# Performance work log

Hardware: AMD Instinct MI355X
Metric: run time of the kernel (lower is better)

The kernel has to match this reference:

```python
import jax, jax.numpy as jnp
import numpy as np
from jax import lax

TAU = 2.0
V_TH = 1.0
SG_ALPHA = 4.0  # spikingjelly default sigmoid surrogate alpha


def lif_multistep(x):
    """Multi-step LIF with hard reset to 0, v_init=0, detach_reset=True.
    x: (T, ...). Returns binary spikes (same shape), with sigmoid surrogate
    gradient injected via straight-through estimator.
    """
    def step(v, xt):
        h = v + (xt - v) / TAU                      # membrane charge
        s_hard = (h >= V_TH).astype(h.dtype)        # heaviside spike
        sur = jax.nn.sigmoid(SG_ALPHA * (h - V_TH))  # surrogate for grad
        s = s_hard + (sur - lax.stop_gradient(sur))  # fwd=hard, bwd=surrogate
        v_next = h * (1.0 - lax.stop_gradient(s))    # hard reset, detached
        return v_next, s
    _, spikes = lax.scan(step, jnp.zeros_like(x[0]), x)
    return spikes


def setup_inputs() -> dict:
    key = jax.random.key(0)
    ks = jax.random.split(key, 6)
    T, B, N, D = 4, 16, 197, 512
    w_std = 1.0 / np.sqrt(D)
    return {
        "x":  jax.random.normal(ks[0], (T, B, N, D), dtype=jnp.float32),
        "Wq": jax.random.normal(ks[1], (D, D), dtype=jnp.float32) * w_std,
        "Wk": jax.random.normal(ks[2], (D, D), dtype=jnp.float32) * w_std,
        "Wv": jax.random.normal(ks[3], (D, D), dtype=jnp.float32) * w_std,
        "Wp": jax.random.normal(ks[4], (D, D), dtype=jnp.float32) * w_std,
        "bp": jnp.zeros((D,), dtype=jnp.float32),
    }


def reference(x, Wq, Wk, Wv, Wp, bp):
    T, B, N, D = x.shape
    H = 8
    dh = D // H
    scale = dh ** -0.5

    # QKV projections (nn.Linear: x @ W.T, no bias)
    q = jnp.einsum('tbnd,ed->tbne', x, Wq)
    k = jnp.einsum('tbnd,ed->tbne', x, Wk)
    v = jnp.einsum('tbnd,ed->tbne', x, Wv)

    # LIF spiking over timestep dim T -> binary spike tensors
    qs = lif_multistep(q).reshape(T, B, N, H, dh).transpose(0, 1, 3, 2, 4)
    ks_ = lif_multistep(k).reshape(T, B, N, H, dh).transpose(0, 1, 3, 2, 4)
    vs = lif_multistep(v).reshape(T, B, N, H, dh).transpose(0, 1, 3, 2, 4)

    # spike-driven attention: binary matmul, no softmax
    attn = jnp.einsum('tbhnd,tbhmd->tbhnm', qs, ks_) * scale  # (T,B,H,N,N)
    attn_map = lax.stop_gradient(attn)
    out = jnp.einsum('tbhnm,tbhmd->tbhnd', attn, vs)          # (T,B,H,N,dh)
    out = out.transpose(0, 1, 3, 2, 4).reshape(T, B, N, D)

    # output projection + LIF
    out = jnp.einsum('tbnd,ed->tbne', out, Wp) + bp
    out = lif_multistep(out)
    return out, attn_map
```

## Files before the change

kernel.cpp:

```cpp
#include <hip/hip_runtime.h>
#include <stdint.h>

#define T_ 4
#define B_ 16
#define N_ 197
#define D_ 512
#define H_ 8
#define DH 64
#define BN_ (B_*N_)
#define PLANE (BN_*D_)
#define M_ (T_*BN_)
#define TENSOR_ELEMS (T_*PLANE)
#define WELEMS (D_*D_)
#define MH (M_*H_)
#define FLAG_TOL 6e-3f
#define NFW3 (3*PLANE/64)
#define NFWP (PLANE/64)

typedef __attribute__((ext_vector_type(8))) short short8v;
typedef __attribute__((ext_vector_type(8))) _Float16 f16x8;
typedef __attribute__((ext_vector_type(4))) float f32x4;
typedef __attribute__((ext_vector_type(16))) float f32x16;
typedef __attribute__((ext_vector_type(4))) unsigned short ushort4v;
typedef unsigned long long u64;
typedef unsigned int u32;

__device__ __forceinline__ ushort f16_bits(float f) {
    _Float16 h = (_Float16)f;
    return __builtin_bit_cast(unsigned short, h);
}
__device__ __forceinline__ float f16_val(ushort u) {
    return (float)__builtin_bit_cast(_Float16, u);
}

__device__ __forceinline__ void gload16(const void* g, void* l) {
    __builtin_amdgcn_global_load_lds(
        (const __attribute__((address_space(1))) unsigned int*)g,
        (__attribute__((address_space(3))) unsigned int*)l, 16, 0, 0);
}

__device__ __forceinline__ short8v unpack8(u32 bits) {
    short8v r;
    #pragma unroll
    for (int j = 0; j < 8; ++j)
        r[j] = (short)(((bits >> j) & 1u) ? 0x3F80 : 0);
    return r;
}

__global__ void cvt16(const float* __restrict__ src, ushort* __restrict__ dst, int n)
{
    int i = (blockIdx.x*256 + threadIdx.x)*4;
    if (i >= n) return;
    float4 v = *(const float4*)(src + i);
    ushort4v o;
    o[0] = f16_bits(v.x); o[1] = f16_bits(v.y);
    o[2] = f16_bits(v.z); o[3] = f16_bits(v.w);
    *(ushort4v*)(dst + i) = o;
}

__global__ __launch_bounds__(256)
void gemm_qkv_lif(const ushort* __restrict__ xh, const ushort* __restrict__ w3h,
                  u64* __restrict__ bits3, u64* __restrict__ fmap3)
{
    __shared__ __align__(16) ushort smem[32768];
    const int tid = threadIdx.x;
    const int lane = tid & 63, wn = tid >> 6;
    const int l31 = lane & 31, lg = lane >> 5;
    const int nyz = 12, nz = 3;

    int nwg = gridDim.x, orig = blockIdx.x;
    int q8 = nwg >> 3, r8 = nwg & 7, xcd = orig & 7, loc = orig >> 3;
    int wg = (xcd < r8 ? xcd*(q8+1) : r8*(q8+1) + (xcd-r8)*q8) + loc;
    int bx = wg / nyz, yz = wg - bx*nyz;
    int by = yz / nz,  z  = yz - by*nz;

    const int bm0 = bx * 32;
    const int bn0 = by * 128;
    const ushort* Wz = w3h + (size_t)z * WELEMS;

    f32x16 acc[4];
    #pragma unroll
    for (int t = 0; t < 4; ++t)
        #pragma unroll
        for (int r = 0; r < 16; ++r) acc[t][r] = 0.f;

    auto STAGE = [&](int buf, int kt) {
        #pragma unroll
        for (int i = 0; i < 8; ++i) {
            const int q = ((i & 3) << 8) | tid;
            const int row = q & 127, c = q >> 7;
            ushort* dst = smem + buf*16384 + ((i >> 2) << 13) + q*8;
            if (i < 4) {
                int t = row >> 5, r32 = row & 31;
                if (bm0 + r32 < BN_)
                    gload16(xh + ((size_t)(t*BN_ + bm0 + r32)*D_ + kt + c*8), dst);
            } else {
                gload16(Wz + ((size_t)(bn0 + row)*D_ + kt + c*8), dst);
            }
        }
    };
    auto COMPUTE = [&](int buf) {
        const ushort* base = smem + buf*16384;
        #pragma unroll
        for (int s = 0; s < 4; ++s) {
            const int cA = (s << 1) | lg;
            f16x8 bv = *(const f16x8*)&base[8192 + (cA*128 + wn*32 + l31)*8];
            #pragma unroll
            for (int t = 0; t < 4; ++t) {
                f16x8 av = *(const f16x8*)&base[(cA*128 + t*32 + l31)*8];
                acc[t] = __builtin_amdgcn_mfma_f32_32x32x16_f16(av, bv, acc[t], 0, 0, 0);
            }
        }
    };

    STAGE(0, 0);
    __syncthreads();
    int cur = 0;
    #pragma unroll
    for (int k64 = 0; k64 < 8; ++k64) {
        if (k64 < 7) STAGE(cur ^ 1, (k64 + 1)*64);
        COMPUTE(cur);
        __syncthreads();
        cur ^= 1;
    }

    u32* sp = (u32*)smem;
    u32* fl = (u32*)smem + 512;
    #pragma unroll
    for (int r = 0; r < 16; ++r) {
        bool s[4]; bool fg = false; float v = 0.f;
        #pragma unroll
        for (int t = 0; t < 4; ++t) {
            float h = v + (acc[t][r] - v)*0.5f;
            s[t] = h >= 1.0f;
            fg |= fabsf(h - 1.0f) < FLAG_TOL;
            v = s[t] ? 0.f : h;
        }
        #pragma unroll
        for (int t = 0; t < 4; ++t) {
            u64 m = __ballot(s[t]);
            if (lane == 0) {
                sp[((wn*4 + t)*16 + r)*2 + 0] = (u32)m;
                sp[((wn*4 + t)*16 + r)*2 + 1] = (u32)(m >> 32);
            }
        }
        u64 fm = __ballot(fg);
        if (lane == 0) {
            fl[(wn*16 + r)*2 + 0] = (u32)fm;
            fl[(wn*16 + r)*2 + 1] = (u32)(fm >> 32);
        }
    }
    __syncthreads();
    {
        int t = tid >> 6, row32 = (tid >> 1) & 31, hl = tid & 1;
        int rr = (row32 & 3) | ((row32 >> 3) << 2);
        int lgg = (row32 >> 2) & 1;
        u64 word = (u64)sp[(((2*hl)*4 + t)*16 + rr)*2 + lgg]
                 | ((u64)sp[(((2*hl+1)*4 + t)*16 + rr)*2 + lgg] << 32);
        if (bm0 + row32 < BN_)
            bits3[(size_t)z*MH + (size_t)(t*BN_ + bm0 + row32)*H_ + (bn0 >> 6) + hl] = word;
        if (tid < 64) {
            int rowf = tid >> 1, hlf = tid & 1;
            int rf = (rowf & 3) | ((rowf >> 3) << 2);
            int lgf = (rowf >> 2) & 1;
            u64 fw = (u64)fl[((2*hlf)*16 + rf)*2 + lgf]
                   | ((u64)fl[((2*hlf+1)*16 + rf)*2 + lgf] << 32);
            if (bm0 + rowf < BN_)
                fmap3[(size_t)z*NFWP + (size_t)(bm0 + rowf)*8 + (bn0 >> 6) + hlf] = fw;
        }
    }
}

__global__ __launch_bounds__(256)
void gemm_proj_lif(const ushort* __restrict__ oh, const ushort* __restrict__ wph,
                   const float* __restrict__ bias, float* __restrict__ outp,
                   u64* __restrict__ fmapp)
{
    __shared__ __align__(16) ushort smem[32768];
    const int tid = threadIdx.x;
    const int lane = tid & 63, wn = tid >> 6;
    const int l31 = lane & 31, lg = lane >> 5;
    const int nyz = 4;

    int nwg = gridDim.x, orig = blockIdx.x;
    int q8 = nwg >> 3, r8 = nwg & 7, xcd = orig & 7, loc = orig >> 3;
    int wg = (xcd < r8 ? xcd*(q8+1) : r8*(q8+1) + (xcd-r8)*q8) + loc;
    int bx = wg / nyz, by = wg - bx*nyz;

    const int bm0 = bx * 32, bn0 = by * 128;

    f32x16 acc[4];
    #pragma unroll
    for (int t = 0; t < 4; ++t)
        #pragma unroll
        for (int r = 0; r < 16; ++r) acc[t][r] = 0.f;

    auto STAGE = [&](int buf, int kt) {
        #pragma unroll
        for (int i = 0; i < 8; ++i) {
            const int q = ((i & 3) << 8) | tid;
            const int row = q & 127, c = q >> 7;
            ushort* dst = smem + buf*16384 + ((i >> 2) << 13) + q*8;
            if (i < 4) {
                int t = row >> 5, r32 = row & 31;
                if (bm0 + r32 < BN_)
                    gload16(oh + ((size_t)(t*BN_ + bm0 + r32)*D_ + kt + c*8), dst);
            } else {
                gload16(wph + ((size_t)(bn0 + row)*D_ + kt + c*8), dst);
            }
        }
    };
    auto COMPUTE = [&](int buf) {
        const ushort* base = smem + buf*16384;
        #pragma unroll
        for (int s = 0; s < 4; ++s) {
            const int cA = (s << 1) | lg;
            f16x8 bv = *(const f16x8*)&base[8192 + (cA*128 + wn*32 + l31)*8];
            #pragma unroll
            for (int t = 0; t < 4; ++t) {
                f16x8 av = *(const f16x8*)&base[(cA*128 + t*32 + l31)*8];
                acc[t] = __builtin_amdgcn_mfma_f32_32x32x16_f16(av, bv, acc[t], 0, 0, 0);
            }
        }
    };

    STAGE(0, 0);
    __syncthreads();
    int cur = 0;
    #pragma unroll
    for (int k64 = 0; k64 < 8; ++k64) {
        if (k64 < 7) STAGE(cur ^ 1, (k64 + 1)*64);
        COMPUTE(cur);
        __syncthreads();
        cur ^= 1;
    }

    const int gcol = bn0 + wn*32 + l31;
    const float bb = bias[gcol];
    u32* fl = (u32*)smem;
    #pragma unroll
    for (int r = 0; r < 16; ++r) {
        const int row32 = (r & 3) + 8*(r >> 2) + 4*lg;
        const bool live = bm0 + row32 < BN_;
        bool fg = false; float v = 0.f;
        #pragma unroll
        for (int t = 0; t < 4; ++t) {
            float h = v + ((acc[t][r] + bb) - v)*0.5f;
            bool st = h >= 1.0f;
            fg |= fabsf(h - 1.0f) < FLAG_TOL;
            if (live)
                outp[(size_t)t*PLANE + (size_t)(bm0 + row32)*D_ + gcol] = st ? 1.0f : 0.0f;
            v = st ? 0.f : h;
        }
        u64 fm = __ballot(fg);
        if (lane == 0) {
            fl[(wn*16 + r)*2 + 0] = (u32)fm;
            fl[(wn*16 + r)*2 + 1] = (u32)(fm >> 32);
        }
    }
    __syncthreads();
    if (tid < 64) {
        int rowf = tid >> 1, hlf = tid & 1;
        int rf = (rowf & 3) | ((rowf >> 3) << 2);
        int lgf = (rowf >> 2) & 1;
        u64 fw = (u64)fl[((2*hlf)*16 + rf)*2 + lgf]
               | ((u64)fl[((2*hlf+1)*16 + rf)*2 + lgf] << 32);
        if (bm0 + rowf < BN_)
            fmapp[(size_t)(bm0 + rowf)*8 + (bn0 >> 6) + hlf] = fw;
    }
}

__global__ __launch_bounds__(256)
void fixup_qkv(const float* __restrict__ x,
               const float* __restrict__ Wq, const float* __restrict__ Wk,
               const float* __restrict__ Wv,
               u64* __restrict__ bits3, const u64* __restrict__ flagmap)
{
    const int lane = threadIdx.x & 63;
    const int wv = blockIdx.x*4 + (threadIdx.x >> 6);
    const int nw = gridDim.x*4;
    for (int w = wv; w < NFW3; w += nw) {
        u64 fm = flagmap[w];
        while (fm) {
            int bit = __ffsll((long long)fm) - 1;
            fm &= fm - 1;
            int id = (w << 6) + bit;
            int tsr = id / PLANE;
            int rem = id - tsr*PLANE;
            int r = rem >> 9, e = rem & (D_-1);
            const float* W = (tsr==0) ? Wq : (tsr==1 ? Wk : Wv);
            const float* wr = W + (size_t)e*D_;
            u64* bits = bits3 + (size_t)tsr*MH;
            float wv8[8];
            #pragma unroll
            for (int i = 0; i < 8; ++i) wv8[i] = wr[lane + 64*i];
            double dots[T_];
            #pragma unroll
            for (int t = 0; t < T_; ++t) {
                const float* xr = x + (size_t)(t*BN_ + r)*D_;
                float xv8[8];
                #pragma unroll
                for (int i = 0; i < 8; ++i) xv8[i] = xr[lane + 64*i];
                double p = 0.0;
                #pragma unroll
                for (int i = 0; i < 8; ++i) p += (double)xv8[i]*(double)wv8[i];
                dots[t] = p;
            }
            #pragma unroll
            for (int off = 32; off > 0; off >>= 1)
                #pragma unroll
                for (int t = 0; t < T_; ++t)
                    dots[t] += __shfl_down(dots[t], off);
            if (lane == 0) {
                double v = 0.0;
                u64 b = 1ull << (e & 63);
                #pragma unroll
                for (int t = 0; t < T_; ++t) {
                    double hh = v + (dots[t] - v)/2.0;
                    bool s = hh >= 1.0;
                    size_t wd = (size_t)(t*BN_ + r)*H_ + (e >> 6);
                    if (s) atomicOr(&bits[wd], b);
                    else   atomicAnd(&bits[wd], ~b);
                    v = s ? 0.0 : hh;
                }
            }
        }
    }
}

#define JP 224
#define VSTR 232

__global__ __launch_bounds__(256)
void attn_fused(const u64* __restrict__ qbits, const u64* __restrict__ kbits,
                const u64* __restrict__ vbits,
                float* __restrict__ attn_out, ushort* __restrict__ of16)
{
    __shared__ ushort Vt[DH][VSTR];
    __shared__ ushort Ss[4][16][VSTR];
    int tb = blockIdx.x, h = blockIdx.y;
    int tid = threadIdx.x, wave = tid >> 6, lane = tid & 63;

    for (int idx = tid; idx < JP*16; idx += 256) {
        int j = idx >> 4, d4 = (idx & 15) << 2;
        ushort vv[4] = {0,0,0,0};
        if (j < N_) {
            u64 vw = vbits[((size_t)tb*N_ + j)*H_ + h];
            #pragma unroll
            for (int r = 0; r < 4; ++r)
                vv[r] = ((vw >> (d4+r)) & 1ull) ? 0x3F80 : 0;
        }
        Vt[d4+0][j]=vv[0]; Vt[d4+1][j]=vv[1]; Vt[d4+2][j]=vv[2]; Vt[d4+3][j]=vv[3];
    }
    for (int idx = lane; idx < 16*16; idx += 64)
        Ss[wave][idx >> 4][208 + (idx & 15)] = 0;
    __syncthreads();

    const int il = lane & 15, kk = (lane >> 4) << 3, ig = (lane >> 4) << 2;
    const size_t amap = ((size_t)tb*H_ + h)*(size_t)(N_*N_);

    for (int it = wave; it < 13; it += 4) {
        int i0 = it << 4;
        int qrow = i0 + il;
        u64 qw = (qrow < N_) ? qbits[((size_t)tb*N_ + qrow)*H_ + h] : 0ull;
        short8v a0 = unpack8((u32)(qw >> kk));
        short8v a1 = unpack8((u32)((qw >> 32) >> kk));
        for (int jt = 0; jt < 13; ++jt) {
            int j0 = jt << 4, jrow = j0 + il;
            u64 kw = (jrow < N_) ? kbits[((size_t)tb*N_ + jrow)*H_ + h] : 0ull;
            short8v b0 = unpack8((u32)(kw >> kk));
            short8v b1 = unpack8((u32)((kw >> 32) >> kk));
            f32x4 c = {0.f, 0.f, 0.f, 0.f};
            c = __builtin_amdgcn_mfma_f32_16x16x32_bf16(a0, b0, c, 0, 0, 0);
            c = __builtin_amdgcn_mfma_f32_16x16x32_bf16(a1, b1, c, 0, 0, 0);
            int j = j0 + il;
            #pragma unroll
            for (int r = 0; r < 4; ++r) {
                float sv = c[r]*0.125f;
                int i = i0 + ig + r;
                if (i < N_ && j < N_)
                    attn_out[amap + (size_t)i*N_ + j] = sv;
                Ss[wave][ig + r][j] = (ushort)(__float_as_uint(sv) >> 16);
            }
        }
        f32x4 o[4];
        #pragma unroll
        for (int dt = 0; dt < 4; ++dt) o[dt] = (f32x4){0.f,0.f,0.f,0.f};
        #pragma unroll
        for (int kt = 0; kt < 7; ++kt) {
            short8v a = *(const short8v*)&Ss[wave][il][kt*32 + kk];
            #pragma unroll
            for (int dt = 0; dt < 4; ++dt) {
                short8v b = *(const short8v*)&Vt[dt*16 + il][kt*32 + kk];
                o[dt] = __builtin_amdgcn_mfma_f32_16x16x32_bf16(a, b, o[dt], 0, 0, 0);
            }
        }
        #pragma unroll
        for (int dt = 0; dt < 4; ++dt)
            #pragma unroll
            for (int r = 0; r < 4; ++r) {
                int i = i0 + ig + r;
                if (i < N_)
                    of16[((size_t)tb*N_ + i)*D_ + (size_t)h*DH + dt*16 + il] =
                        f16_bits(o[dt][r]);
            }
    }
}

__global__ __launch_bounds__(256)
void fixup_proj(const ushort* __restrict__ of16, const float* __restrict__ Wp,
                const float* __restrict__ bp, float* __restrict__ outp,
                const u64* __restrict__ flagmap)
{
    const int lane = threadIdx.x & 63;
    const int wv = blockIdx.x*4 + (threadIdx.x >> 6);
    const int nw = gridDim.x*4;
    for (int w = wv; w < NFWP; w += nw) {
        u64 fm = flagmap[w];
        while (fm) {
            int bit = __ffsll((long long)fm) - 1;
            fm &= fm - 1;
            int rem = (w << 6) + bit;
            int r = rem >> 9, e = rem & (D_-1);
            const float* wr = Wp + (size_t)e*D_;
            float wv8[8];
            #pragma unroll
            for (int i = 0; i < 8; ++i) wv8[i] = wr[lane + 64*i];
            double dots[T_];
            #pragma unroll
            for (int t = 0; t < T_; ++t) {
                const ushort* ar = of16 + (size_t)(t*BN_ + r)*D_;
                float av8[8];
                #pragma unroll
                for (int i = 0; i < 8; ++i) av8[i] = f16_val(ar[lane + 64*i]);
                double p = 0.0;
                #pragma unroll
                for (int i = 0; i < 8; ++i) p += (double)av8[i]*(double)wv8[i];
                dots[t] = p;
            }
            #pragma unroll
            for (int off = 32; off > 0; off >>= 1)
                #pragma unroll
                for (int t = 0; t < T_; ++t)
                    dots[t] += __shfl_down(dots[t], off);
            if (lane == 0) {
                double v = 0.0;
                #pragma unroll
                for (int t = 0; t < T_; ++t) {
                    double xt = dots[t] + (double)bp[e];
                    double h = v + (xt - v)/2.0;
                    bool s = h >= 1.0;
                    outp[(size_t)t*PLANE + rem] = s ? 1.0f : 0.0f;
                    v = s ? 0.0 : h;
                }
            }
        }
    }
}

extern "C" void kernel_launch(void* const* d_in, const int* in_sizes, int n_in,
                              void* d_out, int out_size, void* d_ws, size_t ws_size,
                              hipStream_t stream)
{
    const float* x  = (const float*)d_in[0];
    const float* Wq = (const float*)d_in[1];
    const float* Wk = (const float*)d_in[2];
    const float* Wv = (const float*)d_in[3];
    const float* Wp = (const float*)d_in[4];
    const float* bp = (const float*)d_in[5];
    float* out_spk  = (float*)d_out;
    float* attn_out = (float*)d_out + TENSOR_ELEMS;

    char* ws = (char*)d_ws;
    const size_t BUFB = (size_t)TENSOR_ELEMS * sizeof(float);
    if (ws_size < 4*BUFB) return;
    ushort* of16 = (ushort*)(ws + 2*BUFB);
    char* r3 = ws + 3*BUFB;
    ushort* xh   = (ushort*)r3;
    ushort* w3h  = (ushort*)(r3 + (13u<<20));
    ushort* wph  = (ushort*)(r3 + (15u<<20));
    u64*    bits3 = (u64*)(r3 + (16u<<20));
    u64*    qbits = bits3;
    u64*    kbits = bits3 + MH;
    u64*    vbits = bits3 + 2*(size_t)MH;
    u64*    fmap3 = (u64*)(r3 + (19u<<20));
    u64*    fmapp = (u64*)(r3 + (20u<<20));

    cvt16<<<TENSOR_ELEMS/1024, 256, 0, stream>>>(x, xh, TENSOR_ELEMS);
    cvt16<<<WELEMS/1024, 256, 0, stream>>>(Wq, w3h,            WELEMS);
    cvt16<<<WELEMS/1024, 256, 0, stream>>>(Wk, w3h +   WELEMS, WELEMS);
    cvt16<<<WELEMS/1024, 256, 0, stream>>>(Wv, w3h + 2*WELEMS, WELEMS);
    cvt16<<<WELEMS/1024, 256, 0, stream>>>(Wp, wph,            WELEMS);

    gemm_qkv_lif<<<99*12, 256, 0, stream>>>(xh, w3h, bits3, fmap3);
    fixup_qkv<<<2048, 256, 0, stream>>>(x, Wq, Wk, Wv, bits3, fmap3);

    attn_fused<<<dim3(T_*B_, H_), 256, 0, stream>>>(
        qbits, kbits, vbits, attn_out, of16);

    gemm_proj_lif<<<99*4, 256, 0, stream>>>(of16, wph, bp, out_spk, fmapp);
    fixup_proj<<<1024, 256, 0, stream>>>(of16, Wp, bp, out_spk, fmapp);
}
```

Baseline: 168.9 us.

## Halve GEMM K-tile for occupancy, merge convert launches, coalesce attention map stores

Both fused GEMM+LIF kernels now stage 32-wide K slices instead of 64-wide ones, halving shared memory, and request 4 blocks per CU through launch bounds. The loop runs twice as many stages, each with more barriers per unit of work. The five fp16 conversion launches are merged into one kernel that picks its source buffer by block index, which removes launch overhead. The attention map is now written from the LDS score tile in row-contiguous, lane-coalesced stores instead of scattered per-fragment stores. This relies on the bf16-truncated scores being exact, which holds because they are binary dot products times 0.125.

Result: faster. 159.7 us (-5.4%).

```diff
diff --git a/kernel.cpp b/kernel.cpp
--- a/kernel.cpp
+++ b/kernel.cpp
@@ -47,10 +47,23 @@
     return r;
 }
 
-__global__ void cvt16(const float* __restrict__ src, ushort* __restrict__ dst, int n)
-{
-    int i = (blockIdx.x*256 + threadIdx.x)*4;
-    if (i >= n) return;
+#define NBX (TENSOR_ELEMS/1024)
+#define NBW (WELEMS/1024)
+
+__global__ void cvt_all(const float* __restrict__ x,  const float* __restrict__ Wq,
+                        const float* __restrict__ Wk, const float* __restrict__ Wv,
+                        const float* __restrict__ Wp,
+                        ushort* __restrict__ xh, ushort* __restrict__ w3h,
+                        ushort* __restrict__ wph)
+{
+    int b = blockIdx.x;
+    const float* src; ushort* dst; int base;
+    if      (b < NBX)         { src = x;  dst = xh;             base = b; }
+    else if (b < NBX + NBW)   { src = Wq; dst = w3h;            base = b - NBX; }
+    else if (b < NBX + 2*NBW) { src = Wk; dst = w3h + WELEMS;   base = b - NBX - NBW; }
+    else if (b < NBX + 3*NBW) { src = Wv; dst = w3h + 2*WELEMS; base = b - NBX - 2*NBW; }
+    else                      { src = Wp; dst = wph;            base = b - NBX - 3*NBW; }
+    int i = (base*256 + threadIdx.x)*4;
     float4 v = *(const float4*)(src + i);
     ushort4v o;
     o[0] = f16_bits(v.x); o[1] = f16_bits(v.y);
@@ -58,11 +71,11 @@
     *(ushort4v*)(dst + i) = o;
 }
 
-__global__ __launch_bounds__(256)
+__global__ __launch_bounds__(256, 4)
 void gemm_qkv_lif(const ushort* __restrict__ xh, const ushort* __restrict__ w3h,
                   u64* __restrict__ bits3, u64* __restrict__ fmap3)
 {
-    __shared__ __align__(16) ushort smem[32768];
+    __shared__ __align__(16) ushort smem[16384];
     const int tid = threadIdx.x;
     const int lane = tid & 63, wn = tid >> 6;
     const int l31 = lane & 31, lg = lane >> 5;
@@ -86,11 +99,11 @@
 
     auto STAGE = [&](int buf, int kt) {
         #pragma unroll
-        for (int i = 0; i < 8; ++i) {
-            const int q = ((i & 3) << 8) | tid;
+        for (int i = 0; i < 4; ++i) {
+            const int q = ((i & 1) << 8) | tid;
             const int row = q & 127, c = q >> 7;
-            ushort* dst = smem + buf*16384 + ((i >> 2) << 13) + q*8;
-            if (i < 4) {
+            ushort* dst = smem + buf*8192 + ((i >> 1) << 12) + q*8;
+            if (i < 2) {
                 int t = row >> 5, r32 = row & 31;
                 if (bm0 + r32 < BN_)
                     gload16(xh + ((size_t)(t*BN_ + bm0 + r32)*D_ + kt + c*8), dst);
@@ -100,11 +113,11 @@
         }
     };
     auto COMPUTE = [&](int buf) {
-        const ushort* base = smem + buf*16384;
-        #pragma unroll
-        for (int s = 0; s < 4; ++s) {
+        const ushort* base = smem + buf*8192;
+        #pragma unroll
+        for (int s = 0; s < 2; ++s) {
             const int cA = (s << 1) | lg;
-            f16x8 bv = *(const f16x8*)&base[8192 + (cA*128 + wn*32 + l31)*8];
+            f16x8 bv = *(const f16x8*)&base[4096 + (cA*128 + wn*32 + l31)*8];
             #pragma unroll
             for (int t = 0; t < 4; ++t) {
                 f16x8 av = *(const f16x8*)&base[(cA*128 + t*32 + l31)*8];
@@ -117,8 +130,8 @@
     __syncthreads();
     int cur = 0;
     #pragma unroll
-    for (int k64 = 0; k64 < 8; ++k64) {
-        if (k64 < 7) STAGE(cur ^ 1, (k64 + 1)*64);
+    for (int k32 = 0; k32 < 16; ++k32) {
+        if (k32 < 15) STAGE(cur ^ 1, (k32 + 1)*32);
         COMPUTE(cur);
         __syncthreads();
         cur ^= 1;
@@ -171,12 +184,12 @@
     }
 }
 
-__global__ __launch_bounds__(256)
+__global__ __launch_bounds__(256, 4)
 void gemm_proj_lif(const ushort* __restrict__ oh, const ushort* __restrict__ wph,
                    const float* __restrict__ bias, float* __restrict__ outp,
                    u64* __restrict__ fmapp)
 {
-    __shared__ __align__(16) ushort smem[32768];
+    __shared__ __align__(16) ushort smem[16384];
     const int tid = threadIdx.x;
     const int lane = tid & 63, wn = tid >> 6;
     const int l31 = lane & 31, lg = lane >> 5;
@@ -197,11 +210,11 @@
 
     auto STAGE = [&](int buf, int kt) {
         #pragma unroll
-        for (int i = 0; i < 8; ++i) {
-            const int q = ((i & 3) << 8) | tid;
+        for (int i = 0; i < 4; ++i) {
+            const int q = ((i & 1) << 8) | tid;
             const int row = q & 127, c = q >> 7;
-            ushort* dst = smem + buf*16384 + ((i >> 2) << 13) + q*8;
-            if (i < 4) {
+            ushort* dst = smem + buf*8192 + ((i >> 1) << 12) + q*8;
+            if (i < 2) {
                 int t = row >> 5, r32 = row & 31;
                 if (bm0 + r32 < BN_)
                     gload16(oh + ((size_t)(t*BN_ + bm0 + r32)*D_ + kt + c*8), dst);
@@ -211,11 +224,11 @@
         }
     };
     auto COMPUTE = [&](int buf) {
-        const ushort* base = smem + buf*16384;
-        #pragma unroll
-        for (int s = 0; s < 4; ++s) {
+        const ushort* base = smem + buf*8192;
+        #pragma unroll
+        for (int s = 0; s < 2; ++s) {
             const int cA = (s << 1) | lg;
-            f16x8 bv = *(const f16x8*)&base[8192 + (cA*128 + wn*32 + l31)*8];
+            f16x8 bv = *(const f16x8*)&base[4096 + (cA*128 + wn*32 + l31)*8];
             #pragma unroll
             for (int t = 0; t < 4; ++t) {
                 f16x8 av = *(const f16x8*)&base[(cA*128 + t*32 + l31)*8];
@@ -228,8 +241,8 @@
     __syncthreads();
     int cur = 0;
     #pragma unroll
-    for (int k64 = 0; k64 < 8; ++k64) {
-        if (k64 < 7) STAGE(cur ^ 1, (k64 + 1)*64);
+    for (int k32 = 0; k32 < 16; ++k32) {
+        if (k32 < 15) STAGE(cur ^ 1, (k32 + 1)*32);
         COMPUTE(cur);
         __syncthreads();
         cur ^= 1;
@@ -377,10 +390,20 @@
             #pragma unroll
             for (int r = 0; r < 4; ++r) {
                 float sv = c[r]*0.125f;
-                int i = i0 + ig + r;
-                if (i < N_ && j < N_)
-                    attn_out[amap + (size_t)i*N_ + j] = sv;
                 Ss[wave][ig + r][j] = (ushort)(__float_as_uint(sv) >> 16);
+            }
+        }
+        #pragma unroll
+        for (int r = 0; r < 16; ++r) {
+            int i = i0 + r;
+            if (i < N_) {
+                #pragma unroll
+                for (int g = 0; g < 4; ++g) {
+                    int col = g*64 + lane;
+                    if (col < N_)
+                        attn_out[amap + (size_t)i*N_ + col] =
+                            __uint_as_float((u32)Ss[wave][r][col] << 16);
+                }
             }
         }
         f32x4 o[4];
@@ -486,11 +509,7 @@
     u64*    fmap3 = (u64*)(r3 + (19u<<20));
     u64*    fmapp = (u64*)(r3 + (20u<<20));
 
-    cvt16<<<TENSOR_ELEMS/1024, 256, 0, stream>>>(x, xh, TENSOR_ELEMS);
-    cvt16<<<WELEMS/1024, 256, 0, stream>>>(Wq, w3h,            WELEMS);
-    cvt16<<<WELEMS/1024, 256, 0, stream>>>(Wk, w3h +   WELEMS, WELEMS);
-    cvt16<<<WELEMS/1024, 256, 0, stream>>>(Wv, w3h + 2*WELEMS, WELEMS);
-    cvt16<<<WELEMS/1024, 256, 0, stream>>>(Wp, wph,            WELEMS);
+    cvt_all<<<NBX + 4*NBW, 256, 0, stream>>>(x, Wq, Wk, Wv, Wp, xh, w3h, wph);
 
     gemm_qkv_lif<<<99*12, 256, 0, stream>>>(xh, w3h, bits3, fmap3);
     fixup_qkv<<<2048, 256, 0, stream>>>(x, Wq, Wk, Wv, bits3, fmap3);
```
